# Optimization experiments

Hardware: AMD Instinct MI355X
Metric: run time of the kernel (lower is better)

Reference implementation:

```python
import jax, jax.numpy as jnp
import numpy as np

HB, WB = 200, 200
X_MIN, X_MAX = -50.0, 50.0
Y_MIN, Y_MAX = -50.0, 50.0


def _nearest_resize(x, Hp, Wp):
    # torch F.interpolate(mode='nearest'): src = floor(dst * in/out)
    Hs, Ws = x.shape[-2], x.shape[-1]
    iy = (jnp.arange(Hp) * (Hs / Hp)).astype(jnp.int32)
    ix = (jnp.arange(Wp) * (Ws / Wp)).astype(jnp.int32)
    return x[..., iy[:, None], ix[None, :]]


def _make_extrinsics(B, T, C):
    # per-camera yaw around ego z, composed with axis permutation ego->cam
    P = np.array([[0.0, -1.0, 0.0], [0.0, 0.0, -1.0], [1.0, 0.0, 0.0]], np.float32)
    mats = np.zeros((C, 4, 4), np.float32)
    for c in range(C):
        a = 2.0 * np.pi * c / C
        Rz = np.array([[np.cos(a), -np.sin(a), 0.0], [np.sin(a), np.cos(a), 0.0], [0.0, 0.0, 1.0]], np.float32)
        mats[c, :3, :3] = P @ Rz
        mats[c, :3, 3] = np.array([0.1 * c, -0.05 * c, 1.5], np.float32)
        mats[c, 3, 3] = 1.0
    return jnp.broadcast_to(jnp.asarray(mats), (B, T, C, 4, 4))


def setup_inputs() -> dict:
    key = jax.random.key(0)
    k1, k2 = jax.random.split(key)
    B, T, C, Cr, Hp, Wp = 2, 2, 6, 64, 32, 88
    H, W = 256, 704
    feats = jax.random.normal(k1, (B, T, C, Cr, Hp, Wp), dtype=jnp.float32)
    depths = jax.random.uniform(k2, (B, T, C, H, W), dtype=jnp.float32) * 59.0 + 1.0
    K = jnp.array([[557.0, 0.0, 352.0], [0.0, 557.0, 128.0], [0.0, 0.0, 1.0]], jnp.float32)
    K_scaled = jnp.broadcast_to(K, (B, T, C, 3, 3))
    T_cam_from_ego = _make_extrinsics(B, T, C)
    return {"feats": feats, "depths": depths, "K_scaled": K_scaled,
            "T_cam_from_ego": T_cam_from_ego, "H": H, "W": W}


def reference(feats, depths, K_scaled, T_cam_from_ego, H, W):
    B, T, C, Cr, Hp, Wp = feats.shape
    rx = (X_MAX - X_MIN) / float(WB)
    ry = (Y_MAX - Y_MIN) / float(HB)
    d = _nearest_resize(depths, Hp, Wp)  # [B,T,C,Hp,Wp]
    # scale intrinsics from (H,W) to (Hp,Wp)
    Sy, Sx = Hp / float(H), Wp / float(W)
    scale = jnp.array([[Sx, 1.0, Sx], [1.0, Sy, Sy], [1.0, 1.0, 1.0]], feats.dtype)
    Kp = K_scaled * scale
    T_ego_from_cam = jnp.linalg.inv(T_cam_from_ego)  # [B,T,C,4,4]
    uu = jnp.arange(Wp, dtype=feats.dtype)[None, :]  # broadcast over Hp
    vv = jnp.arange(Hp, dtype=feats.dtype)[:, None]
    fx = Kp[..., 0, 0][..., None, None]
    fy = Kp[..., 1, 1][..., None, None]
    cx = Kp[..., 0, 2][..., None, None]
    cy = Kp[..., 1, 2][..., None, None]
    x_c = (uu - cx) / fx * d
    y_c = (vv - cy) / fy * d
    Xc = jnp.stack([x_c, y_c, d, jnp.ones_like(d)], axis=3)  # [B,T,C,4,Hp,Wp]
    Xe = jnp.einsum('btcij,btcjhw->btcihw', T_ego_from_cam[..., 0:3, :], Xc)
    x = Xe[:, :, :, 0]
    y = Xe[:, :, :, 1]
    valid = (d > 0) & (x >= X_MIN) & (x < X_MAX) & (y >= Y_MIN) & (y < Y_MAX)
    ix = jnp.clip(jnp.floor((x - X_MIN) / rx), 0, WB - 1).astype(jnp.int32)
    iy = jnp.clip(jnp.floor((y - Y_MIN) / ry), 0, HB - 1).astype(jnp.int32)
    lin = iy * WB + ix  # [B,T,C,Hp,Wp]
    idx = jnp.where(valid, lin, 0)
    N, P = B * T * C, Hp * Wp
    seg = (jnp.arange(N, dtype=jnp.int32)[:, None] * (HB * WB) + idx.reshape(N, P)).reshape(-1)
    w = valid.reshape(N, 1, P).astype(feats.dtype)
    vals = (feats.reshape(N, Cr, P) * w).transpose(0, 2, 1).reshape(N * P, Cr)
    out = jax.ops.segment_sum(vals, seg, num_segments=N * HB * WB)  # [N*HB*WB, Cr]
    cnt = jax.ops.segment_sum(w.reshape(-1), seg, num_segments=N * HB * WB)
    out = out.reshape(B, T, C, HB * WB, Cr)
    cnt = cnt.reshape(B, T, C, HB * WB)
    num = out.sum(axis=2)                                  # [B,T,HB*WB,Cr]
    den = jnp.maximum(cnt, 1.0).sum(axis=2)                # [B,T,HB*WB]
    res = num / den[..., None]
    return res.transpose(0, 1, 3, 2).reshape(B, T, Cr, HB, WB)
```

## Files before the change

kernel.cpp:

```cpp
#include <hip/hip_runtime.h>

constexpr int B  = 2, T = 2, C = 6, Cr = 64, Hp = 32, Wp = 88;
constexpr int H  = 256, W = 704;
constexpr int HB = 200, WB = 200;
constexpr int NB   = B * T * C;
constexpr int BT   = B * T;
constexpr int P    = Hp * Wp;
constexpr int NBIN = HB * WB;
constexpr int PTS_BT = C * P;

constexpr float X_MIN = -50.f, Y_MIN = -50.f;

constexpr int TB     = 64;
constexpr int TILES  = NBIN / TB;
constexpr int NBUCK  = BT * TILES;

constexpr size_t CNT_BYTES   = (size_t)NB * NBIN * 4;
constexpr size_t TCNT_BYTES  = (size_t)NBUCK * 4;
constexpr size_t OFF_BYTES   = (size_t)NBUCK * 4;
constexpr size_t CUR_BYTES   = (size_t)NBUCK * 4;
constexpr size_t BIDX_BYTES  = (size_t)NB * P * 4;
constexpr size_t REC_BYTES   = (size_t)NB * P * 4;

__global__ void geom_kernel(const float* __restrict__ depths,
                            const float* __restrict__ Kmat,
                            const float* __restrict__ Tmat,
                            int* __restrict__ binidx,
                            int* __restrict__ cnt,
                            int* __restrict__ tilecnt) {
    const int n = blockIdx.y;
    const int p = blockIdx.x * blockDim.x + threadIdx.x;
    const int v = p / Wp, u = p % Wp;

    const float* Kp = Kmat + n * 9;
    const float* M  = Tmat + n * 16;

    const float Sx = (float)Wp / (float)W;
    const float Sy = (float)Hp / (float)H;
    const float fx = Kp[0] * Sx, cx = Kp[2] * Sx;
    const float fy = Kp[4] * Sy, cy = Kp[5] * Sy;

    const float r00 = M[0], t0 = M[3];
    const float r10 = M[4], t1 = M[7];
    const float r20 = M[8], t2 = M[11];
    const float r01 = M[1], r11 = M[5], r21 = M[9];
    const float ti0 = -(r00 * t0 + r10 * t1 + r20 * t2);
    const float ti1 = -(r01 * t0 + r11 * t1 + r21 * t2);

    const float d = depths[(size_t)n * H * W + (size_t)(v * (H / Hp)) * W + u * (W / Wp)];

    const float xc = ((float)u - cx) / fx * d;
    const float yc = ((float)v - cy) / fy * d;
    const float x  = r00 * xc + r10 * yc + r20 * d + ti0;
    const float y  = r01 * xc + r11 * yc + r21 * d + ti1;

    const bool valid = (d > 0.f) && (x >= X_MIN) && (x < -X_MIN) &&
                       (y >= Y_MIN) && (y < -Y_MIN);
    int bin = -1;
    if (valid) {
        const float ixf = floorf((x - X_MIN) * 2.f);
        const float iyf = floorf((y - Y_MIN) * 2.f);
        const int ix = (int)fminf(fmaxf(ixf, 0.f), (float)(WB - 1));
        const int iy = (int)fminf(fmaxf(iyf, 0.f), (float)(HB - 1));
        bin = iy * WB + ix;
        atomicAdd(&cnt[n * NBIN + bin], 1);
        atomicAdd(&tilecnt[(n / C) * TILES + (bin >> 6)], 1);
    }
    binidx[n * P + p] = bin;
}

__global__ void scan_kernel(const int* __restrict__ tilecnt,
                            int* __restrict__ off,
                            int* __restrict__ cursor) {
    __shared__ int part[256];
    const int t = threadIdx.x;
    constexpr int CH = (NBUCK + 255) / 256;
    int pre[CH];
    int s = 0;
#pragma unroll
    for (int k = 0; k < CH; ++k) {
        const int i = t * CH + k;
        pre[k] = s;
        if (i < NBUCK) s += tilecnt[i];
    }
    part[t] = s;
    __syncthreads();
    for (int dlt = 1; dlt < 256; dlt <<= 1) {
        const int v = (t >= dlt) ? part[t - dlt] : 0;
        __syncthreads();
        part[t] += v;
        __syncthreads();
    }
    const int excl = (t == 0) ? 0 : part[t - 1];
#pragma unroll
    for (int k = 0; k < CH; ++k) {
        const int i = t * CH + k;
        if (i < NBUCK) {
            const int o = excl + pre[k];
            off[i] = o;
            cursor[i] = o;
        }
    }
}

__global__ void fill_kernel(const int* __restrict__ binidx,
                            int* __restrict__ cursor,
                            int* __restrict__ rec) {
    const int n = blockIdx.y;
    const int p = blockIdx.x * blockDim.x + threadIdx.x;
    const int b = binidx[n * P + p];
    if (b >= 0) {
        const int bt  = n / C;
        const int pbt = (n % C) * P + p;
        const int pos = atomicAdd(&cursor[bt * TILES + (b >> 6)], 1);
        rec[pos] = (pbt << 6) | (b & 63);
    }
}

__global__ void transpose_kernel(const float* __restrict__ feats,
                                 float* __restrict__ feats_t) {
    __shared__ float tile[64][65];
    const int n  = blockIdx.y;
    const int p0 = blockIdx.x * 64;
    const int tp = threadIdx.x & 63;
    const int tq = threadIdx.x >> 6;

    const float* src = feats + (size_t)n * Cr * P + p0;
#pragma unroll
    for (int k = 0; k < 16; ++k) {
        const int cr = k * 4 + tq;
        tile[cr][tp] = src[(size_t)cr * P + tp];
    }
    __syncthreads();
    float* dst = feats_t + ((size_t)n * P + p0) * Cr;
#pragma unroll
    for (int k = 0; k < 16; ++k) {
        const int p = k * 4 + tq;
        dst[(size_t)p * Cr + tp] = tile[tp][p];
    }
}

__global__ void accum_kernel(const float* __restrict__ feats_t,
                             const int* __restrict__ rec,
                             const int* __restrict__ off,
                             const int* __restrict__ cursor,
                             const int* __restrict__ cnt,
                             float* __restrict__ out) {
    __shared__ float acc[TB * 64];
    const int bt   = blockIdx.y;
    const int tile = blockIdx.x;
    const int lo   = tile * TB;

    for (int i = threadIdx.x; i < TB * 64; i += 256) acc[i] = 0.f;
    __syncthreads();

    const int lane = threadIdx.x & 63;
    const int wave = threadIdx.x >> 6;
    const int bucket = bt * TILES + tile;
    const int start = off[bucket];
    const int end   = cursor[bucket];
    const float* f  = feats_t + (size_t)bt * PTS_BT * Cr;

    for (int j = start + wave; j < end; j += 4) {
        const int r  = rec[j];
        const int bl = r & 63;
        const int p  = r >> 6;
        const float v = f[(size_t)p * Cr + lane];
        atomicAdd(&acc[bl * 64 + (lane ^ (bl & 31))], v);
    }
    __syncthreads();

    const int bin = lo + lane;
    float den = 0.f;
#pragma unroll
    for (int c = 0; c < C; ++c) {
        const int cc = cnt[(bt * C + c) * NBIN + bin];
        den += (float)(cc > 1 ? cc : 1);
    }
    const float rden = 1.f / den;
    float* ob = out + (size_t)bt * Cr * NBIN + bin;
#pragma unroll
    for (int k = 0; k < 16; ++k) {
        const int cr = wave * 16 + k;
        ob[(size_t)cr * NBIN] = acc[lane * 64 + (cr ^ (lane & 31))] * rden;
    }
}

extern "C" void kernel_launch(void* const* d_in, const int* in_sizes, int n_in,
                              void* d_out, int out_size, void* d_ws, size_t ws_size,
                              hipStream_t stream) {
    const float* feats  = (const float*)d_in[0];
    const float* depths = (const float*)d_in[1];
    const float* Kmat   = (const float*)d_in[2];
    const float* Tmat   = (const float*)d_in[3];

    char* w = (char*)d_ws;
    int*   cnt     = (int*)w;                      w += CNT_BYTES;
    int*   tilecnt = (int*)w;                      w += TCNT_BYTES;
    int*   off     = (int*)w;                      w += OFF_BYTES;
    int*   cursor  = (int*)w;                      w += CUR_BYTES;
    int*   binidx  = (int*)w;                      w += BIDX_BYTES;
    int*   rec     = (int*)w;                      w += REC_BYTES;
    float* feats_t = (float*)w;
    float* out     = (float*)d_out;

    hipMemsetAsync(cnt, 0, CNT_BYTES + TCNT_BYTES, stream);

    geom_kernel<<<dim3(P / 256, NB), 256, 0, stream>>>(depths, Kmat, Tmat,
                                                       binidx, cnt, tilecnt);
    scan_kernel<<<1, 256, 0, stream>>>(tilecnt, off, cursor);
    fill_kernel<<<dim3(P / 256, NB), 256, 0, stream>>>(binidx, cursor, rec);
    transpose_kernel<<<dim3(P / 64, NB), 256, 0, stream>>>(feats, feats_t);
    accum_kernel<<<dim3(TILES, BT), 256, 0, stream>>>(feats_t, rec, off,
                                                      cursor, cnt, out);
}
```

Before: 164.5 us.

## Fuse fill with transpose into CSR-ordered features and count per-camera bins in LDS

Merges the fill and transpose kernels so each point's transposed feature row is written directly to its sorted bucket position, and accum then reads features contiguously instead of gathering. It drops the large per-camera bin count array, its memset and the global atomics on it. Per-camera counts are now taken in shared memory inside accum from a camera id packed into the metadata. The cost is scattered 256-byte row writes in the fill stage and one extra shared atomic per record.

```diff
diff --git a/kernel.cpp b/kernel.cpp
--- a/kernel.cpp
+++ b/kernel.cpp
@@ -7,7 +7,7 @@
 constexpr int BT   = B * T;
 constexpr int P    = Hp * Wp;
 constexpr int NBIN = HB * WB;
-constexpr int PTS_BT = C * P;
+constexpr int NPTS = NB * P;
 
 constexpr float X_MIN = -50.f, Y_MIN = -50.f;
 
@@ -15,18 +15,16 @@
 constexpr int TILES  = NBIN / TB;
 constexpr int NBUCK  = BT * TILES;
 
-constexpr size_t CNT_BYTES   = (size_t)NB * NBIN * 4;
-constexpr size_t TCNT_BYTES  = (size_t)NBUCK * 4;
-constexpr size_t OFF_BYTES   = (size_t)NBUCK * 4;
-constexpr size_t CUR_BYTES   = (size_t)NBUCK * 4;
-constexpr size_t BIDX_BYTES  = (size_t)NB * P * 4;
-constexpr size_t REC_BYTES   = (size_t)NB * P * 4;
+constexpr size_t TCNT_BYTES = (size_t)NBUCK * 4;
+constexpr size_t OFF_BYTES  = (size_t)NBUCK * 4;
+constexpr size_t CUR_BYTES  = (size_t)NBUCK * 4;
+constexpr size_t BIDX_BYTES = (size_t)NPTS * 4;
+constexpr size_t META_BYTES = (size_t)NPTS * 4;
 
 __global__ void geom_kernel(const float* __restrict__ depths,
                             const float* __restrict__ Kmat,
                             const float* __restrict__ Tmat,
                             int* __restrict__ binidx,
-                            int* __restrict__ cnt,
                             int* __restrict__ tilecnt) {
     const int n = blockIdx.y;
     const int p = blockIdx.x * blockDim.x + threadIdx.x;
@@ -63,7 +61,6 @@
         const int ix = (int)fminf(fmaxf(ixf, 0.f), (float)(WB - 1));
         const int iy = (int)fminf(fmaxf(iyf, 0.f), (float)(HB - 1));
         bin = iy * WB + ix;
-        atomicAdd(&cnt[n * NBIN + bin], 1);
         atomicAdd(&tilecnt[(n / C) * TILES + (bin >> 6)], 1);
     }
     binidx[n * P + p] = bin;
@@ -103,55 +100,57 @@
     }
 }
 
-__global__ void fill_kernel(const int* __restrict__ binidx,
-                            int* __restrict__ cursor,
-                            int* __restrict__ rec) {
-    const int n = blockIdx.y;
-    const int p = blockIdx.x * blockDim.x + threadIdx.x;
-    const int b = binidx[n * P + p];
-    if (b >= 0) {
-        const int bt  = n / C;
-        const int pbt = (n % C) * P + p;
-        const int pos = atomicAdd(&cursor[bt * TILES + (b >> 6)], 1);
-        rec[pos] = (pbt << 6) | (b & 63);
-    }
-}
-
-__global__ void transpose_kernel(const float* __restrict__ feats,
-                                 float* __restrict__ feats_t) {
+__global__ void fillT_kernel(const float* __restrict__ feats,
+                             const int* __restrict__ binidx,
+                             int* __restrict__ cursor,
+                             int* __restrict__ meta,
+                             float* __restrict__ csr_feat) {
     __shared__ float tile[64][65];
-    const int n  = blockIdx.y;
-    const int p0 = blockIdx.x * 64;
-    const int tp = threadIdx.x & 63;
-    const int tq = threadIdx.x >> 6;
-
+    __shared__ int posArr[64];
+    const int n    = blockIdx.y;
+    const int p0   = blockIdx.x * 64;
+    const int t    = threadIdx.x;
+    const int lane = t & 63, wq = t >> 6;
+    const int bt = n / C, c = n % C;
+
+    if (t < 64) {
+        const int b = binidx[n * P + p0 + t];
+        int pos = -1;
+        if (b >= 0) {
+            pos = atomicAdd(&cursor[bt * TILES + (b >> 6)], 1);
+            meta[pos] = (b & 63) | (c << 6);
+        }
+        posArr[t] = pos;
+    }
     const float* src = feats + (size_t)n * Cr * P + p0;
 #pragma unroll
     for (int k = 0; k < 16; ++k) {
-        const int cr = k * 4 + tq;
-        tile[cr][tp] = src[(size_t)cr * P + tp];
-    }
-    __syncthreads();
-    float* dst = feats_t + ((size_t)n * P + p0) * Cr;
+        const int cr = k * 4 + wq;
+        tile[cr][lane] = src[(size_t)cr * P + lane];
+    }
+    __syncthreads();
 #pragma unroll
     for (int k = 0; k < 16; ++k) {
-        const int p = k * 4 + tq;
-        dst[(size_t)p * Cr + tp] = tile[tp][p];
-    }
-}
-
-__global__ void accum_kernel(const float* __restrict__ feats_t,
-                             const int* __restrict__ rec,
+        const int pt  = wq * 16 + k;
+        const int pos = posArr[pt];
+        if (pos >= 0)
+            csr_feat[(size_t)pos * 64 + lane] = tile[lane][pt];
+    }
+}
+
+__global__ void accum_kernel(const float* __restrict__ csr_feat,
+                             const int* __restrict__ meta,
                              const int* __restrict__ off,
                              const int* __restrict__ cursor,
-                             const int* __restrict__ cnt,
                              float* __restrict__ out) {
     __shared__ float acc[TB * 64];
+    __shared__ int cntc[TB * 9];
     const int bt   = blockIdx.y;
     const int tile = blockIdx.x;
     const int lo   = tile * TB;
 
     for (int i = threadIdx.x; i < TB * 64; i += 256) acc[i] = 0.f;
+    for (int i = threadIdx.x; i < TB * 9; i += 256) cntc[i] = 0;
     __syncthreads();
 
     const int lane = threadIdx.x & 63;
@@ -159,14 +158,13 @@
     const int bucket = bt * TILES + tile;
     const int start = off[bucket];
     const int end   = cursor[bucket];
-    const float* f  = feats_t + (size_t)bt * PTS_BT * Cr;
 
     for (int j = start + wave; j < end; j += 4) {
-        const int r  = rec[j];
-        const int bl = r & 63;
-        const int p  = r >> 6;
-        const float v = f[(size_t)p * Cr + lane];
+        const int m  = meta[j];
+        const int bl = m & 63;
+        const float v = csr_feat[(size_t)j * 64 + lane];
         atomicAdd(&acc[bl * 64 + (lane ^ (bl & 31))], v);
+        if (lane == 0) atomicAdd(&cntc[bl * 9 + (m >> 6)], 1);
     }
     __syncthreads();
 
@@ -174,15 +172,15 @@
     float den = 0.f;
 #pragma unroll
     for (int c = 0; c < C; ++c) {
-        const int cc = cnt[(bt * C + c) * NBIN + bin];
+        const int cc = cntc[lane * 9 + c];
         den += (float)(cc > 1 ? cc : 1);
     }
-    const float rden = 1.f / den;
+    const float r = 1.f / den;
     float* ob = out + (size_t)bt * Cr * NBIN + bin;
 #pragma unroll
     for (int k = 0; k < 16; ++k) {
         const int cr = wave * 16 + k;
-        ob[(size_t)cr * NBIN] = acc[lane * 64 + (cr ^ (lane & 31))] * rden;
+        ob[(size_t)cr * NBIN] = acc[lane * 64 + (cr ^ (lane & 31))] * r;
     }
 }
 
@@ -195,22 +193,21 @@
     const float* Tmat   = (const float*)d_in[3];
 
     char* w = (char*)d_ws;
-    int*   cnt     = (int*)w;                      w += CNT_BYTES;
-    int*   tilecnt = (int*)w;                      w += TCNT_BYTES;
-    int*   off     = (int*)w;                      w += OFF_BYTES;
-    int*   cursor  = (int*)w;                      w += CUR_BYTES;
-    int*   binidx  = (int*)w;                      w += BIDX_BYTES;
-    int*   rec     = (int*)w;                      w += REC_BYTES;
-    float* feats_t = (float*)w;
-    float* out     = (float*)d_out;
-
-    hipMemsetAsync(cnt, 0, CNT_BYTES + TCNT_BYTES, stream);
+    int*   tilecnt  = (int*)w;   w += TCNT_BYTES;
+    int*   off      = (int*)w;   w += OFF_BYTES;
+    int*   cursor   = (int*)w;   w += CUR_BYTES;
+    int*   binidx   = (int*)w;   w += BIDX_BYTES;
+    int*   meta     = (int*)w;   w += META_BYTES;
+    float* csr_feat = (float*)w;
+    float* out      = (float*)d_out;
+
+    hipMemsetAsync(tilecnt, 0, TCNT_BYTES, stream);
 
     geom_kernel<<<dim3(P / 256, NB), 256, 0, stream>>>(depths, Kmat, Tmat,
-                                                       binidx, cnt, tilecnt);
+                                                       binidx, tilecnt);
     scan_kernel<<<1, 256, 0, stream>>>(tilecnt, off, cursor);
-    fill_kernel<<<dim3(P / 256, NB), 256, 0, stream>>>(binidx, cursor, rec);
-    transpose_kernel<<<dim3(P / 64, NB), 256, 0, stream>>>(feats, feats_t);
-    accum_kernel<<<dim3(TILES, BT), 256, 0, stream>>>(feats_t, rec, off,
-                                                      cursor, cnt, out);
-}
+    fillT_kernel<<<dim3(P / 64, NB), 256, 0, stream>>>(feats, binidx, cursor,
+                                                       meta, csr_feat);
+    accum_kernel<<<dim3(TILES, BT), 256, 0, stream>>>(csr_feat, meta, off,
+                                                      cursor, out);
+}
```

Result: no change. 162.1 us (-1.5%).
